# Performance work log

Measured on AMD Instinct MI355X. Metric: run time of the kernel, lower is better.

The kernel has to match this reference:

```python
import jax, jax.numpy as jnp
import numpy as np

N_NODES = 100000
N_EDGES = 1600000
D_NODE = 32
D_EDGE = 16
D_HID = 64
D_OUT = 32


def setup_inputs() -> dict:
    key = jax.random.key(0)
    ks = jax.random.split(key, 7)
    x = jax.random.normal(ks[0], (N_NODES, D_NODE), dtype=jnp.float32)
    edge_index = jax.random.randint(ks[1], (2, N_EDGES), 0, N_NODES, dtype=jnp.int64)
    edge_attr = jax.random.normal(ks[2], (N_EDGES, D_EDGE), dtype=jnp.float32)
    # 2-layer MLP params (Linear -> ReLU -> Linear), He-ish scaling
    W1 = jax.random.normal(ks[3], (D_NODE + D_EDGE, D_HID), dtype=jnp.float32) * (2.0 / (D_NODE + D_EDGE)) ** 0.5
    b1 = jnp.zeros((D_HID,), dtype=jnp.float32)
    W2 = jax.random.normal(ks[4], (D_HID, D_OUT), dtype=jnp.float32) * (2.0 / D_HID) ** 0.5
    b2 = jnp.zeros((D_OUT,), dtype=jnp.float32)
    return {"x": x, "edge_index": edge_index, "edge_attr": edge_attr,
            "W1": W1, "b1": b1, "W2": W2, "b2": b2}


def reference(x, edge_index, edge_attr, W1, b1, W2, b2):
    row, col = edge_index[0], edge_index[1]
    # gather source-node feats and concat with edge feats: [E, d_node + d_edge]
    inp = jnp.concatenate([x[col], edge_attr], axis=1)
    # 2-layer MLP over edges
    h = jax.nn.relu(inp @ W1 + b1)
    messages = h @ W2 + b2  # [E, d_out]
    # scatter-sum aggregate by destination node
    message = jax.ops.segment_sum(messages, row, num_segments=x.shape[0])
    return message
```

## Files before the change

kernel.cpp:

```cpp
#include <hip/hip_runtime.h>
#include <hip/hip_bf16.h>
#include <stdint.h>

#define N_NODES 100000
#define N_EDGES 1600000
#define D_NODE  32
#define D_EDGE  16
#define D_IN    48
#define D_HID   64
#define D_OUT   32

#define NFLAGS_OFF  ((size_t)0)
#define NB1_OFF     ((size_t)64)
#define NB2_OFF     ((size_t)320)
#define W1BF_OFF    ((size_t)1024)
#define W2BF_OFF    ((size_t)9216)
#define COUNTS_OFF  ((size_t)65536)
#define OFFSETS_OFF ((size_t)466944)
#define GCUR_OFF    ((size_t)917504)
#define BLKSUM_OFF  ((size_t)1048576)
#define TMP_OFF     ((size_t)2097152)
#define REC_OFF     ((size_t)20971520)
#define ACCUM_OFF   ((size_t)41943040)

#define SCAN_NB 391
#define EDGE_NB (N_EDGES / 256)

#define NBKT 98
#define BCAP 20480
#define S1_EDGES 2048
#define S1_NB 782

typedef __attribute__((ext_vector_type(8))) short bf16x8;
typedef __attribute__((ext_vector_type(4))) float f32x4;

__device__ inline float bf2f(unsigned int u16) {
    return __uint_as_float(u16 << 16);
}
__device__ inline unsigned short f2bf_rne(float f) {
    unsigned int x = __float_as_uint(f);
    unsigned int r = (x + 0x7FFFu + ((x >> 16) & 1u)) >> 16;
    return (unsigned short)r;
}
__device__ inline unsigned int pk_bf2(float a, float b) {
    float2 f; f.x = a; f.y = b;
    __hip_bfloat162 h = __float22bfloat162_rn(f);
    return *reinterpret_cast<unsigned int*>(&h);
}
__device__ inline float ld_f(const void* p, int i, int isbf) {
    if (isbf) return bf2f(((const unsigned short*)p)[i]);
    return ((const float*)p)[i];
}
__device__ inline bf16x8 pack_bf8(float4 v0, float4 v1) {
    union { unsigned int u[4]; bf16x8 v; } r;
    r.u[0] = pk_bf2(v0.x, v0.y);
    r.u[1] = pk_bf2(v0.z, v0.w);
    r.u[2] = pk_bf2(v1.x, v1.y);
    r.u[3] = pk_bf2(v1.z, v1.w);
    return r.v;
}

__global__ __launch_bounds__(256) void prep_kernel(
        const void* __restrict__ xq, const void* __restrict__ idxq,
        const void* __restrict__ W1q, const void* __restrict__ b1q,
        const void* __restrict__ W2q, const void* __restrict__ b2q,
        char* __restrict__ ws) {
    const int t = threadIdx.x;
    const int i0 = blockIdx.x * 256 + t;
    int* counts = (int*)(ws + COUNTS_OFF);
    if (i0 < N_NODES) counts[i0] = 0;

    float4* acc4 = (float4*)(ws + ACCUM_OFF);
    float4 z; z.x = z.y = z.z = z.w = 0.0f;
    for (int i = i0; i < N_NODES * 32 / 4; i += SCAN_NB * 256) acc4[i] = z;

    if (blockIdx.x != 0) return;

    if (t < NBKT) ((int*)(ws + GCUR_OFF))[t] = t * BCAP;

    __shared__ int s_isbf;
    if (t < 64) {
        unsigned short u = ((const unsigned short*)xq)[t];
        unsigned long long mb = __ballot(((u >> 7) & 0xFF) >= 140);
        int wodd = ((const int*)idxq)[2 * t + 1];
        unsigned long long mi = __ballot(wodd != 0);
        if (t == 0) {
            int* flags = (int*)(ws + NFLAGS_OFF);
            flags[0] = (mb == 0ULL);
            flags[1] = (mi == 0ULL);
            s_isbf = (mb == 0ULL);
        }
    }
    __syncthreads();
    const int isbf = s_isbf;
    float* b1 = (float*)(ws + NB1_OFF);
    float* b2 = (float*)(ws + NB2_OFF);
    unsigned short* w1b = (unsigned short*)(ws + W1BF_OFF);
    unsigned short* w2b = (unsigned short*)(ws + W2BF_OFF);

    if (t < D_HID) b1[t] = ld_f(b1q, t, isbf);
    if (t < D_OUT) b2[t] = ld_f(b2q, t, isbf);

    for (int i = t; i < D_HID * 64; i += 256) {
        int n = i >> 6, k = i & 63;
        float v = (k < D_IN) ? ld_f(W1q, k * D_HID + n, isbf) : 0.0f;
        w1b[i] = f2bf_rne(v);
    }
    for (int i = t; i < D_OUT * 64; i += 256) {
        int n = i >> 6, k = i & 63;
        w2b[i] = f2bf_rne(ld_f(W2q, k * D_OUT + n, isbf));
    }
}

__global__ __launch_bounds__(256) void bucket_kernel(const void* __restrict__ idxq,
                                                     char* __restrict__ ws) {
    const int is64 = ((const int*)(ws + NFLAGS_OFF))[1];
    __shared__ int hist[NBKT];
    __shared__ int base[NBKT];
    __shared__ int lcur[NBKT];
    const int t = threadIdx.x;
    if (t < NBKT) hist[t] = 0;
    __syncthreads();

    const int e0 = blockIdx.x * S1_EDGES;
    int dstv[8], srcv[8];
#pragma unroll
    for (int i = 0; i < 8; ++i) {
        const int e = e0 + i * 256 + t;
        int dst = -1, src = 0;
        if (e < N_EDGES) {
            if (is64) {
                const long long* ip = (const long long*)idxq;
                dst = (int)ip[e];
                src = (int)ip[N_EDGES + e];
            } else {
                const int* ip = (const int*)idxq;
                dst = ip[e];
                src = ip[N_EDGES + e];
            }
            atomicAdd((int*)(ws + COUNTS_OFF) + dst, 1);
            atomicAdd(&hist[dst >> 10], 1);
        }
        dstv[i] = dst; srcv[i] = src;
    }
    __syncthreads();
    if (t < NBKT) {
        base[t] = atomicAdd((int*)(ws + GCUR_OFF) + t, hist[t]);
        lcur[t] = 0;
    }
    __syncthreads();

    unsigned long long* tmp = (unsigned long long*)(ws + TMP_OFF);
#pragma unroll
    for (int i = 0; i < 8; ++i) {
        const int e = e0 + i * 256 + t;
        if (e < N_EDGES) {
            const int b = dstv[i] >> 10;
            const int r = atomicAdd(&lcur[b], 1);
            unsigned long long rec = (unsigned long long)(unsigned)srcv[i]
                                   | ((unsigned long long)(unsigned)e       << 17)
                                   | ((unsigned long long)(unsigned)dstv[i] << 38);
            tmp[(size_t)base[b] + r] = rec;
        }
    }
}

__global__ __launch_bounds__(1024) void sort_kernel(char* __restrict__ ws) {
    __shared__ int lcur[1024];
    const int b = blockIdx.x;
    const int t = threadIdx.x;
    lcur[t] = 0;
    __syncthreads();

    const int n0 = b << 10;
    const int cnt = ((const int*)(ws + GCUR_OFF))[b] - b * BCAP;
    const unsigned long long* tmp = (const unsigned long long*)(ws + TMP_OFF) + (size_t)b * BCAP;
    unsigned long long* rec = (unsigned long long*)(ws + REC_OFF);
    const int* offs = (const int*)(ws + OFFSETS_OFF);

    for (int i = t; i < cnt; i += 1024) {
        unsigned long long r = tmp[i];
        const int dst = (int)(r >> 38);
        const int rk = atomicAdd(&lcur[dst - n0], 1);
        rec[(size_t)offs[dst] + rk] = r;
    }
}

__global__ __launch_bounds__(256) void scan_block_kernel(char* __restrict__ ws) {
    __shared__ int s[256];
    const int* counts = (const int*)(ws + COUNTS_OFF);
    int* offs   = (int*)(ws + OFFSETS_OFF);
    int* blksum = (int*)(ws + BLKSUM_OFF);
    const int t = threadIdx.x;
    const int i = blockIdx.x * 256 + t;
    int v = (i < N_NODES) ? counts[i] : 0;
    s[t] = v;
    __syncthreads();
    for (int d = 1; d < 256; d <<= 1) {
        int a = (t >= d) ? s[t - d] : 0;
        __syncthreads();
        s[t] += a;
        __syncthreads();
    }
    if (i < N_NODES) offs[i] = s[t] - v;
    if (t == 255) blksum[blockIdx.x] = s[255];
}

__global__ __launch_bounds__(256) void scan_add_kernel(char* __restrict__ ws) {
    __shared__ int s[256];
    int* offs = (int*)(ws + OFFSETS_OFF);
    const int* blksum = (const int*)(ws + BLKSUM_OFF);
    const int t = threadIdx.x;
    const int b = blockIdx.x;
    int acc = 0;
    for (int j = t; j < b; j += 256) acc += blksum[j];
    s[t] = acc;
    __syncthreads();
    for (int d = 128; d > 0; d >>= 1) {
        if (t < d) s[t] += s[t + d];
        __syncthreads();
    }
    const int prefix = s[0];
    const int i = b * 256 + t;
    if (i < N_NODES) offs[i] += prefix;
    if (i == 0) offs[N_NODES] = N_EDGES;
}

__global__ __launch_bounds__(256) void edge_mlp_agg_kernel(
        const void* __restrict__ xq,
        const void* __restrict__ eaq,
        const char* __restrict__ wsro,
        float* __restrict__ accum) {
    const int isbf = ((const int*)(wsro + NFLAGS_OFF))[0];

    __shared__ __align__(16) unsigned short hbuf[4][2][16][72];

    const int w   = threadIdx.x >> 6;
    const int l   = threadIdx.x & 63;
    const int m16 = l & 15;
    const int q   = l >> 4;

    const unsigned short* w1b = (const unsigned short*)(wsro + W1BF_OFF);
    const unsigned short* w2b = (const unsigned short*)(wsro + W2BF_OFF);
    const float* b1 = (const float*)(wsro + NB1_OFF);
    const float* b2 = (const float*)(wsro + NB2_OFF);
    const unsigned long long* rec = (const unsigned long long*)(wsro + REC_OFF);

    bf16x8 w1f[4][2], w2f[2][2];
#pragma unroll
    for (int t = 0; t < 4; ++t)
#pragma unroll
        for (int c = 0; c < 2; ++c)
            w1f[t][c] = *(const bf16x8*)(w1b + ((t * 16 + m16) * 64 + c * 32 + q * 8));
#pragma unroll
    for (int t = 0; t < 2; ++t)
#pragma unroll
        for (int c = 0; c < 2; ++c)
            w2f[t][c] = *(const bf16x8*)(w2b + ((t * 16 + m16) * 64 + c * 32 + q * 8));

    const int kb = blockIdx.x * 256 + w * 64;

    int srcv[4], ev[4], dstv[4];
#pragma unroll
    for (int g = 0; g < 4; ++g) {
        unsigned long long r = rec[kb + g * 16 + m16];
        srcv[g] = (int)(r & 0x1FFFFULL);
        ev[g]   = (int)((r >> 17) & 0x1FFFFFULL);
        dstv[g] = (int)(r >> 38);
    }

    bf16x8 A0[4], A1[4];
#pragma unroll
    for (int g = 0; g < 4; ++g) {
        if (isbf) {
            const unsigned short* x  = (const unsigned short*)xq;
            const unsigned short* ea = (const unsigned short*)eaq;
            A0[g] = *(const bf16x8*)(x + (size_t)srcv[g] * D_NODE + q * 8);
            A1[g] = *(const bf16x8*)(ea + (size_t)ev[g] * D_EDGE + (q & 1) * 8);
        } else {
            const float* x  = (const float*)xq;
            const float* ea = (const float*)eaq;
            const float4* xp = (const float4*)(x + (size_t)srcv[g] * D_NODE + q * 8);
            A0[g] = pack_bf8(xp[0], xp[1]);
            const float4* ap = (const float4*)(ea + (size_t)ev[g] * D_EDGE + (q & 1) * 8);
            A1[g] = pack_bf8(ap[0], ap[1]);
        }
    }

    const float b1v[4] = { b1[m16], b1[16 + m16], b1[32 + m16], b1[48 + m16] };
    const float b2v[2] = { b2[m16], b2[16 + m16] };

    auto L1 = [&](int g, int b) {
#pragma unroll
        for (int t = 0; t < 4; ++t) {
            f32x4 c;
            c[0] = c[1] = c[2] = c[3] = b1v[t];
            c = __builtin_amdgcn_mfma_f32_16x16x32_bf16(A0[g], w1f[t][0], c, 0, 0, 0);
            c = __builtin_amdgcn_mfma_f32_16x16x32_bf16(A1[g], w1f[t][1], c, 0, 0, 0);
            unsigned int u0 = pk_bf2(fmaxf(c[0], 0.0f), fmaxf(c[1], 0.0f));
            unsigned int u1 = pk_bf2(fmaxf(c[2], 0.0f), fmaxf(c[3], 0.0f));
            hbuf[w][b][q * 4 + 0][t * 16 + m16] = (unsigned short)u0;
            hbuf[w][b][q * 4 + 1][t * 16 + m16] = (unsigned short)(u0 >> 16);
            hbuf[w][b][q * 4 + 2][t * 16 + m16] = (unsigned short)u1;
            hbuf[w][b][q * 4 + 3][t * 16 + m16] = (unsigned short)(u1 >> 16);
        }
    };

    auto L2R = [&](int g, int b) {
        bf16x8 a20 = *(const bf16x8*)(&hbuf[w][b][m16][q * 8]);
        bf16x8 a21 = *(const bf16x8*)(&hbuf[w][b][m16][32 + q * 8]);
        f32x4 c0, c1;
        c0[0] = c0[1] = c0[2] = c0[3] = b2v[0];
        c1[0] = c1[1] = c1[2] = c1[3] = b2v[1];
        c0 = __builtin_amdgcn_mfma_f32_16x16x32_bf16(a20, w2f[0][0], c0, 0, 0, 0);
        c0 = __builtin_amdgcn_mfma_f32_16x16x32_bf16(a21, w2f[0][1], c0, 0, 0, 0);
        c1 = __builtin_amdgcn_mfma_f32_16x16x32_bf16(a20, w2f[1][0], c1, 0, 0, 0);
        c1 = __builtin_amdgcn_mfma_f32_16x16x32_bf16(a21, w2f[1][1], c1, 0, 0, 0);

        const int dstw = dstv[g];
        int dprev = __shfl(dstw, (m16 + 15) & 15, 16);
        bool isStart = (m16 == 0) || (dprev != dstw);
        unsigned long long bal = __ballot(isStart);
        unsigned mask16 = (unsigned)(bal >> (l & 48)) & 0xFFFFu;
        int start = 0;
        while (start < 16) {
            unsigned rest = mask16 >> 1 >> start;
            int next = rest ? (start + 1 + (int)__builtin_ctz(rest)) : 16;
            int d = __shfl(dstw, start, 16);
            float s0 = 0.0f, s1 = 0.0f;
#pragma unroll
            for (int r = 0; r < 4; ++r) {
                int m = q * 4 + r;
                bool in = (m >= start) && (m < next);
                s0 += in ? c0[r] : 0.0f;
                s1 += in ? c1[r] : 0.0f;
            }
            s0 += __shfl_xor(s0, 16); s0 += __shfl_xor(s0, 32);
            s1 += __shfl_xor(s1, 16); s1 += __shfl_xor(s1, 32);
            if (q == 0) {
                unsafeAtomicAdd(accum + (size_t)d * 32 + m16,      s0);
                unsafeAtomicAdd(accum + (size_t)d * 32 + 16 + m16, s1);
            }
            start = next;
        }
    };

    L1(0, 0);
    L1(1, 1);
    L2R(0, 0);
    L1(2, 0);
    L2R(1, 1);
    L1(3, 1);
    L2R(2, 0);
    L2R(3, 1);
}

__global__ __launch_bounds__(256) void convert_kernel(
        const char* __restrict__ wsro, const float* __restrict__ accum,
        void* __restrict__ out) {
    const int isbf = ((const int*)(wsro + NFLAGS_OFF))[0];
    const int i = blockIdx.x * 256 + threadIdx.x;
    float4 v = ((const float4*)accum)[i];
    if (isbf) {
        uint2 u;
        u.x = pk_bf2(v.x, v.y);
        u.y = pk_bf2(v.z, v.w);
        ((uint2*)out)[i] = u;
    } else {
        ((float4*)out)[i] = v;
    }
}

extern "C" void kernel_launch(void* const* d_in, const int* in_sizes, int n_in,
                              void* d_out, int out_size, void* d_ws, size_t ws_size,
                              hipStream_t stream) {
    const void* x   = d_in[0];
    const void* idx = d_in[1];
    const void* ea  = d_in[2];
    const void* W1  = d_in[3];
    const void* b1  = d_in[4];
    const void* W2  = d_in[5];
    const void* b2  = d_in[6];
    char* ws = (char*)d_ws;

    hipLaunchKernelGGL(prep_kernel, dim3(SCAN_NB), dim3(256), 0, stream,
                       x, idx, W1, b1, W2, b2, ws);

    hipLaunchKernelGGL(bucket_kernel, dim3(S1_NB), dim3(256), 0, stream, idx, ws);

    hipLaunchKernelGGL(scan_block_kernel, dim3(SCAN_NB), dim3(256), 0, stream, ws);
    hipLaunchKernelGGL(scan_add_kernel,   dim3(SCAN_NB), dim3(256), 0, stream, ws);

    hipLaunchKernelGGL(sort_kernel, dim3(NBKT), dim3(1024), 0, stream, ws);

    hipLaunchKernelGGL(edge_mlp_agg_kernel, dim3(EDGE_NB), dim3(256), 0, stream,
                       x, ea, (const char*)ws, (float*)(ws + ACCUM_OFF));

    hipLaunchKernelGGL(convert_kernel, dim3(N_NODES * 32 / 4 / 256), dim3(256), 0, stream,
                       (const char*)ws, (const float*)(ws + ACCUM_OFF), d_out);
}
```

Before: 378.9 us.

## Drop global counting sort; bucket-local sort with pre-converted bf16 x and edge_attr

Removes the global per-node count atomics and the two scan kernels. Each bucket now builds its own histogram and scan in shared memory, and records store bucket-local indices. The partition pass also converts edge_attr to bf16 and writes it in bucket order, and the prep pass converts x to bf16 once, so the MLP kernel does fewer random fp32 gathers and no per-element conversion. The MLP grid becomes per-bucket slices with padding and early exit, which adds idle blocks and an extra write of the reordered edge features. It also relies on each bucket's edge count fitting in a smaller fixed capacity.

```diff
diff --git a/kernel.cpp b/kernel.cpp
--- a/kernel.cpp
+++ b/kernel.cpp
@@ -10,26 +10,24 @@
 #define D_HID   64
 #define D_OUT   32
 
+#define NBKT 98
+#define BCAP 18432
+#define SLICES (BCAP / 256)
+#define S1_EDGES 2048
+#define S1_NB 782
+#define SCAN_NB 391
+
 #define NFLAGS_OFF  ((size_t)0)
 #define NB1_OFF     ((size_t)64)
 #define NB2_OFF     ((size_t)320)
 #define W1BF_OFF    ((size_t)1024)
 #define W2BF_OFF    ((size_t)9216)
-#define COUNTS_OFF  ((size_t)65536)
-#define OFFSETS_OFF ((size_t)466944)
-#define GCUR_OFF    ((size_t)917504)
-#define BLKSUM_OFF  ((size_t)1048576)
-#define TMP_OFF     ((size_t)2097152)
-#define REC_OFF     ((size_t)20971520)
-#define ACCUM_OFF   ((size_t)41943040)
-
-#define SCAN_NB 391
-#define EDGE_NB (N_EDGES / 256)
-
-#define NBKT 98
-#define BCAP 20480
-#define S1_EDGES 2048
-#define S1_NB 782
+#define GCUR_OFF    ((size_t)16384)
+#define XBF_OFF     ((size_t)65536)
+#define TMPH_OFF    ((size_t)8388608)
+#define TMPE_OFF    ((size_t)16777216)
+#define REC_OFF     ((size_t)75497472)
+#define ACCUM_OFF   ((size_t)90177536)
 
 typedef __attribute__((ext_vector_type(8))) short bf16x8;
 typedef __attribute__((ext_vector_type(4))) float f32x4;
@@ -50,14 +48,6 @@
 __device__ inline float ld_f(const void* p, int i, int isbf) {
     if (isbf) return bf2f(((const unsigned short*)p)[i]);
     return ((const float*)p)[i];
-}
-__device__ inline bf16x8 pack_bf8(float4 v0, float4 v1) {
-    union { unsigned int u[4]; bf16x8 v; } r;
-    r.u[0] = pk_bf2(v0.x, v0.y);
-    r.u[1] = pk_bf2(v0.z, v0.w);
-    r.u[2] = pk_bf2(v1.x, v1.y);
-    r.u[3] = pk_bf2(v1.z, v1.w);
-    return r.v;
 }
 
 __global__ __launch_bounds__(256) void prep_kernel(
@@ -67,32 +57,48 @@
         char* __restrict__ ws) {
     const int t = threadIdx.x;
     const int i0 = blockIdx.x * 256 + t;
-    int* counts = (int*)(ws + COUNTS_OFF);
-    if (i0 < N_NODES) counts[i0] = 0;
-
-    float4* acc4 = (float4*)(ws + ACCUM_OFF);
-    float4 z; z.x = z.y = z.z = z.w = 0.0f;
-    for (int i = i0; i < N_NODES * 32 / 4; i += SCAN_NB * 256) acc4[i] = z;
-
-    if (blockIdx.x != 0) return;
-
-    if (t < NBKT) ((int*)(ws + GCUR_OFF))[t] = t * BCAP;
 
     __shared__ int s_isbf;
     if (t < 64) {
         unsigned short u = ((const unsigned short*)xq)[t];
         unsigned long long mb = __ballot(((u >> 7) & 0xFF) >= 140);
+        if (t == 0) s_isbf = (mb == 0ULL);
+    }
+
+    float4* acc4 = (float4*)(ws + ACCUM_OFF);
+    float4 z; z.x = z.y = z.z = z.w = 0.0f;
+    for (int i = i0; i < (N_NODES + 1) * 32 / 4; i += SCAN_NB * 256) acc4[i] = z;
+
+    __syncthreads();
+    const int isbf = s_isbf;
+
+    unsigned short* xbf = (unsigned short*)(ws + XBF_OFF);
+    for (int i = i0; i < N_NODES * 32 / 8; i += SCAN_NB * 256) {
+        uint4 o;
+        if (isbf) {
+            o = ((const uint4*)xq)[i];
+        } else {
+            const float4* xp = (const float4*)xq + i * 2;
+            float4 a = xp[0], b = xp[1];
+            o.x = pk_bf2(a.x, a.y); o.y = pk_bf2(a.z, a.w);
+            o.z = pk_bf2(b.x, b.y); o.w = pk_bf2(b.z, b.w);
+        }
+        ((uint4*)xbf)[i] = o;
+    }
+
+    if (blockIdx.x != 0) return;
+
+    if (t < NBKT) ((int*)(ws + GCUR_OFF))[t] = t * BCAP;
+    if (t < 64) {
         int wodd = ((const int*)idxq)[2 * t + 1];
         unsigned long long mi = __ballot(wodd != 0);
         if (t == 0) {
             int* flags = (int*)(ws + NFLAGS_OFF);
-            flags[0] = (mb == 0ULL);
+            flags[0] = isbf;
             flags[1] = (mi == 0ULL);
-            s_isbf = (mb == 0ULL);
-        }
-    }
-    __syncthreads();
-    const int isbf = s_isbf;
+        }
+    }
+
     float* b1 = (float*)(ws + NB1_OFF);
     float* b2 = (float*)(ws + NB2_OFF);
     unsigned short* w1b = (unsigned short*)(ws + W1BF_OFF);
@@ -112,9 +118,11 @@
     }
 }
 
-__global__ __launch_bounds__(256) void bucket_kernel(const void* __restrict__ idxq,
-                                                     char* __restrict__ ws) {
+__global__ __launch_bounds__(256) void partition_kernel(
+        const void* __restrict__ idxq, const void* __restrict__ eaq,
+        char* __restrict__ ws) {
     const int is64 = ((const int*)(ws + NFLAGS_OFF))[1];
+    const int isbf = ((const int*)(ws + NFLAGS_OFF))[0];
     __shared__ int hist[NBKT];
     __shared__ int base[NBKT];
     __shared__ int lcur[NBKT];
@@ -123,25 +131,17 @@
     __syncthreads();
 
     const int e0 = blockIdx.x * S1_EDGES;
-    int dstv[8], srcv[8];
+    int dstv[8];
 #pragma unroll
     for (int i = 0; i < 8; ++i) {
         const int e = e0 + i * 256 + t;
-        int dst = -1, src = 0;
+        int dst = -1;
         if (e < N_EDGES) {
-            if (is64) {
-                const long long* ip = (const long long*)idxq;
-                dst = (int)ip[e];
-                src = (int)ip[N_EDGES + e];
-            } else {
-                const int* ip = (const int*)idxq;
-                dst = ip[e];
-                src = ip[N_EDGES + e];
-            }
-            atomicAdd((int*)(ws + COUNTS_OFF) + dst, 1);
+            if (is64) dst = (int)((const long long*)idxq)[e];
+            else      dst = ((const int*)idxq)[e];
             atomicAdd(&hist[dst >> 10], 1);
         }
-        dstv[i] = dst; srcv[i] = src;
+        dstv[i] = dst;
     }
     __syncthreads();
     if (t < NBKT) {
@@ -150,88 +150,85 @@
     }
     __syncthreads();
 
-    unsigned long long* tmp = (unsigned long long*)(ws + TMP_OFF);
+    unsigned int*   tmph = (unsigned int*)(ws + TMPH_OFF);
+    unsigned short* tmpe = (unsigned short*)(ws + TMPE_OFF);
 #pragma unroll
     for (int i = 0; i < 8; ++i) {
         const int e = e0 + i * 256 + t;
-        if (e < N_EDGES) {
-            const int b = dstv[i] >> 10;
-            const int r = atomicAdd(&lcur[b], 1);
-            unsigned long long rec = (unsigned long long)(unsigned)srcv[i]
-                                   | ((unsigned long long)(unsigned)e       << 17)
-                                   | ((unsigned long long)(unsigned)dstv[i] << 38);
-            tmp[(size_t)base[b] + r] = rec;
+        if (e >= N_EDGES) continue;
+        const int dst = dstv[i];
+        int src;
+        if (is64) src = (int)((const long long*)idxq)[N_EDGES + e];
+        else      src = ((const int*)idxq)[N_EDGES + e];
+        const int b = dst >> 10;
+        const int r = atomicAdd(&lcur[b], 1);
+        const size_t slot = (size_t)base[b] + r;
+
+        tmph[slot] = (unsigned)src | ((unsigned)(dst & 1023) << 17);
+
+        uint4 u;
+        if (isbf) {
+            const uint4* p = (const uint4*)((const unsigned short*)eaq + (size_t)e * 16);
+            u = p[0];
+            ((uint4*)(tmpe + slot * 16))[0] = u;
+            u = p[1];
+            ((uint4*)(tmpe + slot * 16))[1] = u;
+        } else {
+            const float4* p = (const float4*)((const float*)eaq + (size_t)e * 16);
+            float4 a = p[0], b4 = p[1], c = p[2], d = p[3];
+            u.x = pk_bf2(a.x, a.y);  u.y = pk_bf2(a.z, a.w);
+            u.z = pk_bf2(b4.x, b4.y); u.w = pk_bf2(b4.z, b4.w);
+            ((uint4*)(tmpe + slot * 16))[0] = u;
+            u.x = pk_bf2(c.x, c.y);  u.y = pk_bf2(c.z, c.w);
+            u.z = pk_bf2(d.x, d.y);  u.w = pk_bf2(d.z, d.w);
+            ((uint4*)(tmpe + slot * 16))[1] = u;
         }
     }
 }
 
 __global__ __launch_bounds__(1024) void sort_kernel(char* __restrict__ ws) {
-    __shared__ int lcur[1024];
+    __shared__ int hist[1024];
+    __shared__ int cur[1024];
     const int b = blockIdx.x;
     const int t = threadIdx.x;
-    lcur[t] = 0;
-    __syncthreads();
-
-    const int n0 = b << 10;
+    hist[t] = 0;
+    __syncthreads();
+
     const int cnt = ((const int*)(ws + GCUR_OFF))[b] - b * BCAP;
-    const unsigned long long* tmp = (const unsigned long long*)(ws + TMP_OFF) + (size_t)b * BCAP;
-    unsigned long long* rec = (unsigned long long*)(ws + REC_OFF);
-    const int* offs = (const int*)(ws + OFFSETS_OFF);
+    const unsigned int* tmph = (const unsigned int*)(ws + TMPH_OFF) + (size_t)b * BCAP;
+    unsigned long long* rec = (unsigned long long*)(ws + REC_OFF) + (size_t)b * BCAP;
+
+    for (int i = t; i < cnt; i += 1024)
+        atomicAdd(&hist[(tmph[i] >> 17) & 1023], 1);
+    __syncthreads();
+
+    int v = hist[t];
+    for (int d = 1; d < 1024; d <<= 1) {
+        int a = (t >= d) ? hist[t - d] : 0;
+        __syncthreads();
+        hist[t] += a;
+        __syncthreads();
+    }
+    cur[t] = hist[t] - v;
+    __syncthreads();
 
     for (int i = t; i < cnt; i += 1024) {
-        unsigned long long r = tmp[i];
-        const int dst = (int)(r >> 38);
-        const int rk = atomicAdd(&lcur[dst - n0], 1);
-        rec[(size_t)offs[dst] + rk] = r;
-    }
-}
-
-__global__ __launch_bounds__(256) void scan_block_kernel(char* __restrict__ ws) {
-    __shared__ int s[256];
-    const int* counts = (const int*)(ws + COUNTS_OFF);
-    int* offs   = (int*)(ws + OFFSETS_OFF);
-    int* blksum = (int*)(ws + BLKSUM_OFF);
-    const int t = threadIdx.x;
-    const int i = blockIdx.x * 256 + t;
-    int v = (i < N_NODES) ? counts[i] : 0;
-    s[t] = v;
-    __syncthreads();
-    for (int d = 1; d < 256; d <<= 1) {
-        int a = (t >= d) ? s[t - d] : 0;
-        __syncthreads();
-        s[t] += a;
-        __syncthreads();
-    }
-    if (i < N_NODES) offs[i] = s[t] - v;
-    if (t == 255) blksum[blockIdx.x] = s[255];
-}
-
-__global__ __launch_bounds__(256) void scan_add_kernel(char* __restrict__ ws) {
-    __shared__ int s[256];
-    int* offs = (int*)(ws + OFFSETS_OFF);
-    const int* blksum = (const int*)(ws + BLKSUM_OFF);
-    const int t = threadIdx.x;
-    const int b = blockIdx.x;
-    int acc = 0;
-    for (int j = t; j < b; j += 256) acc += blksum[j];
-    s[t] = acc;
-    __syncthreads();
-    for (int d = 128; d > 0; d >>= 1) {
-        if (t < d) s[t] += s[t + d];
-        __syncthreads();
-    }
-    const int prefix = s[0];
-    const int i = b * 256 + t;
-    if (i < N_NODES) offs[i] += prefix;
-    if (i == 0) offs[N_NODES] = N_EDGES;
+        unsigned int h = tmph[i];
+        const int rd = (h >> 17) & 1023;
+        const int rk = atomicAdd(&cur[rd], 1);
+        unsigned long long out = ((unsigned long long)rd << 32)
+                               | ((unsigned long long)(unsigned)i << 17)
+                               | (h & 0x1FFFFu);
+        rec[rk] = out;
+    }
 }
 
 __global__ __launch_bounds__(256) void edge_mlp_agg_kernel(
-        const void* __restrict__ xq,
-        const void* __restrict__ eaq,
         const char* __restrict__ wsro,
         float* __restrict__ accum) {
-    const int isbf = ((const int*)(wsro + NFLAGS_OFF))[0];
+    const int b = blockIdx.y;
+    const int cnt = ((const int*)(wsro + GCUR_OFF))[b] - b * BCAP;
+    if (blockIdx.x * 256 >= cnt) return;
 
     __shared__ __align__(16) unsigned short hbuf[4][2][16][72];
 
@@ -244,7 +241,9 @@
     const unsigned short* w2b = (const unsigned short*)(wsro + W2BF_OFF);
     const float* b1 = (const float*)(wsro + NB1_OFF);
     const float* b2 = (const float*)(wsro + NB2_OFF);
-    const unsigned long long* rec = (const unsigned long long*)(wsro + REC_OFF);
+    const unsigned short* xbf  = (const unsigned short*)(wsro + XBF_OFF);
+    const unsigned short* tmpe = (const unsigned short*)(wsro + TMPE_OFF) + (size_t)b * BCAP * 16;
+    const unsigned long long* rec = (const unsigned long long*)(wsro + REC_OFF) + (size_t)b * BCAP;
 
     bf16x8 w1f[4][2], w2f[2][2];
 #pragma unroll
@@ -259,38 +258,36 @@
             w2f[t][c] = *(const bf16x8*)(w2b + ((t * 16 + m16) * 64 + c * 32 + q * 8));
 
     const int kb = blockIdx.x * 256 + w * 64;
-
-    int srcv[4], ev[4], dstv[4];
+    const int n0 = b << 10;
+
+    int srcv[4], tixv[4], dstv[4];
 #pragma unroll
     for (int g = 0; g < 4; ++g) {
-        unsigned long long r = rec[kb + g * 16 + m16];
-        srcv[g] = (int)(r & 0x1FFFFULL);
-        ev[g]   = (int)((r >> 17) & 0x1FFFFFULL);
-        dstv[g] = (int)(r >> 38);
+        const int p = kb + g * 16 + m16;
+        unsigned long long r = rec[p];
+        if (p < cnt) {
+            unsigned int lo = (unsigned int)r;
+            srcv[g] = (int)(lo & 0x1FFFFu);
+            tixv[g] = (int)(lo >> 17);
+            dstv[g] = n0 + (int)(r >> 32);
+        } else {
+            srcv[g] = 0;
+            tixv[g] = 0;
+            dstv[g] = N_NODES;
+        }
     }
 
     bf16x8 A0[4], A1[4];
 #pragma unroll
     for (int g = 0; g < 4; ++g) {
-        if (isbf) {
-            const unsigned short* x  = (const unsigned short*)xq;
-            const unsigned short* ea = (const unsigned short*)eaq;
-            A0[g] = *(const bf16x8*)(x + (size_t)srcv[g] * D_NODE + q * 8);
-            A1[g] = *(const bf16x8*)(ea + (size_t)ev[g] * D_EDGE + (q & 1) * 8);
-        } else {
-            const float* x  = (const float*)xq;
-            const float* ea = (const float*)eaq;
-            const float4* xp = (const float4*)(x + (size_t)srcv[g] * D_NODE + q * 8);
-            A0[g] = pack_bf8(xp[0], xp[1]);
-            const float4* ap = (const float4*)(ea + (size_t)ev[g] * D_EDGE + (q & 1) * 8);
-            A1[g] = pack_bf8(ap[0], ap[1]);
-        }
+        A0[g] = *(const bf16x8*)(xbf  + (size_t)srcv[g] * D_NODE + q * 8);
+        A1[g] = *(const bf16x8*)(tmpe + (size_t)tixv[g] * 16 + (q & 1) * 8);
     }
 
     const float b1v[4] = { b1[m16], b1[16 + m16], b1[32 + m16], b1[48 + m16] };
     const float b2v[2] = { b2[m16], b2[16 + m16] };
 
-    auto L1 = [&](int g, int b) {
+    auto L1 = [&](int g, int bb) {
 #pragma unroll
         for (int t = 0; t < 4; ++t) {
             f32x4 c;
@@ -299,16 +296,16 @@
             c = __builtin_amdgcn_mfma_f32_16x16x32_bf16(A1[g], w1f[t][1], c, 0, 0, 0);
             unsigned int u0 = pk_bf2(fmaxf(c[0], 0.0f), fmaxf(c[1], 0.0f));
             unsigned int u1 = pk_bf2(fmaxf(c[2], 0.0f), fmaxf(c[3], 0.0f));
-            hbuf[w][b][q * 4 + 0][t * 16 + m16] = (unsigned short)u0;
-            hbuf[w][b][q * 4 + 1][t * 16 + m16] = (unsigned short)(u0 >> 16);
-            hbuf[w][b][q * 4 + 2][t * 16 + m16] = (unsigned short)u1;
-            hbuf[w][b][q * 4 + 3][t * 16 + m16] = (unsigned short)(u1 >> 16);
+            hbuf[w][bb][q * 4 + 0][t * 16 + m16] = (unsigned short)u0;
+            hbuf[w][bb][q * 4 + 1][t * 16 + m16] = (unsigned short)(u0 >> 16);
+            hbuf[w][bb][q * 4 + 2][t * 16 + m16] = (unsigned short)u1;
+            hbuf[w][bb][q * 4 + 3][t * 16 + m16] = (unsigned short)(u1 >> 16);
         }
     };
 
-    auto L2R = [&](int g, int b) {
-        bf16x8 a20 = *(const bf16x8*)(&hbuf[w][b][m16][q * 8]);
-        bf16x8 a21 = *(const bf16x8*)(&hbuf[w][b][m16][32 + q * 8]);
+    auto L2R = [&](int g, int bb) {
+        bf16x8 a20 = *(const bf16x8*)(&hbuf[w][bb][m16][q * 8]);
+        bf16x8 a21 = *(const bf16x8*)(&hbuf[w][bb][m16][32 + q * 8]);
         f32x4 c0, c1;
         c0[0] = c0[1] = c0[2] = c0[3] = b2v[0];
         c1[0] = c1[1] = c1[2] = c1[3] = b2v[1];
@@ -386,15 +383,12 @@
     hipLaunchKernelGGL(prep_kernel, dim3(SCAN_NB), dim3(256), 0, stream,
                        x, idx, W1, b1, W2, b2, ws);
 
-    hipLaunchKernelGGL(bucket_kernel, dim3(S1_NB), dim3(256), 0, stream, idx, ws);
-
-    hipLaunchKernelGGL(scan_block_kernel, dim3(SCAN_NB), dim3(256), 0, stream, ws);
-    hipLaunchKernelGGL(scan_add_kernel,   dim3(SCAN_NB), dim3(256), 0, stream, ws);
+    hipLaunchKernelGGL(partition_kernel, dim3(S1_NB), dim3(256), 0, stream, idx, ea, ws);
 
     hipLaunchKernelGGL(sort_kernel, dim3(NBKT), dim3(1024), 0, stream, ws);
 
-    hipLaunchKernelGGL(edge_mlp_agg_kernel, dim3(EDGE_NB), dim3(256), 0, stream,
-                       x, ea, (const char*)ws, (float*)(ws + ACCUM_OFF));
+    hipLaunchKernelGGL(edge_mlp_agg_kernel, dim3(SLICES, NBKT), dim3(256), 0, stream,
+                       (const char*)ws, (float*)(ws + ACCUM_OFF));
 
     hipLaunchKernelGGL(convert_kernel, dim3(N_NODES * 32 / 4 / 256), dim3(256), 0, stream,
                        (const char*)ws, (const float*)(ws + ACCUM_OFF), d_out);
```

Result: faster. 371.3 us (-2.0%).
